# Kernel optimization log

Hardware: AMD Instinct MI355X
Metric: run time of the kernel (lower is better)

## Reference

```python
import jax, jax.numpy as jnp
import numpy as np
from jax import lax

H = 1024
D = 128
T = 64  # n_step + n_middle


def gru_cell(x, h, w_ih, w_hh, b_ih, b_hh):
    # torch.nn.GRUCell gate order: r, z, n
    gi = x @ w_ih.T + b_ih
    gh = h @ w_hh.T + b_hh
    ir, iz, i_n = jnp.split(gi, 3, axis=-1)
    hr, hz, h_n = jnp.split(gh, 3, axis=-1)
    r = jax.nn.sigmoid(ir + hr)
    z = jax.nn.sigmoid(iz + hz)
    n = jnp.tanh(i_n + r * h_n)
    return (1.0 - z) * n + z * h


def decoder(z_seq, z8, n1, w_init, b_init, wi1, wh1, bi1, bh1, wi2, wh2, bi2, bh2, w_out, b_out):
    B = z_seq.shape[0]
    out0 = jnp.zeros((B, D), z_seq.dtype).at[:, -1].set(1.0)
    h0 = z8 @ w_init.T + b_init              # [B, H]
    h1 = jnp.zeros_like(h0)                  # replaced at i == 0
    xs = (jnp.arange(T), jnp.swapaxes(z_seq, 0, 1))  # ([T], [T, B, D])

    def step(carry, x):
        h0, h1, out = carry
        i, z_i = x
        inp = jnp.where(i <= n1 - 1, z_i, out)
        h0n = gru_cell(inp, h0, wi1, wh1, bi1, bh1)
        h1 = jnp.where(i == 0, h0n, h1)
        h1n = gru_cell(h0n, h1, wi2, wh2, bi2, bh2)
        out = h1n @ w_out.T + b_out          # [B, 128]
        return (h0n, h1n, out), out

    _, outs = lax.scan(step, (h0, h1, out0), xs)  # [T, B, 128]
    return jnp.swapaxes(outs[n1 - 1:], 0, 1)      # [B, T-n1+1, 128]


def _p(key, shape):
    return jax.random.normal(key, shape, dtype=jnp.float32) * 0.02


def setup_inputs() -> dict:
    key = jax.random.key(0)
    ks = jax.random.split(key, 32)
    B = 2048
    inp = {
        'zp': jax.random.normal(ks[0], (B, T, D), jnp.float32),
        'zr': jax.random.normal(ks[1], (B, T, D), jnp.float32),
        'zp8': jax.random.normal(ks[2], (B, D), jnp.float32),
        'zr8': jax.random.normal(ks[3], (B, D), jnp.float32),
        'n1': 16,
        'n2': 48,
    }
    # GRU cells 1..4: (w_ih [3H, in], w_hh [3H, H], b_ih [3H], b_hh [3H])
    for j, name in enumerate(['1', '2', '3', '4']):
        in_dim = D if name in ('1', '3') else H
        inp['wi' + name] = _p(ks[4 + 4 * j], (3 * H, in_dim))
        inp['wh' + name] = _p(ks[5 + 4 * j], (3 * H, H))
        inp['bi' + name] = _p(ks[6 + 4 * j], (3 * H,))
        inp['bh' + name] = _p(ks[7 + 4 * j], (3 * H,))
    inp['w_init0'] = _p(ks[20], (H, D)); inp['b_init0'] = _p(ks[21], (H,))
    inp['w_init1'] = _p(ks[22], (H, D)); inp['b_init1'] = _p(ks[23], (H,))
    inp['w_out0'] = _p(ks[24], (D, H)); inp['b_out0'] = _p(ks[25], (D,))
    inp['w_out1'] = _p(ks[26], (D, H)); inp['b_out1'] = _p(ks[27], (D,))
    return inp


def reference(zp, zr, zp8, zr8, n1, n2,
              wi1, wh1, bi1, bh1, wi2, wh2, bi2, bh2,
              wi3, wh3, bi3, bh3, wi4, wh4, bi4, bh4,
              w_init0, b_init0, w_init1, b_init1,
              w_out0, b_out0, w_out1, b_out1):
    z_r = decoder(zr, zr8, n1, w_init0, b_init0, wi1, wh1, bi1, bh1,
                  wi2, wh2, bi2, bh2, w_out0, b_out0)
    z_p = decoder(zp, zp8, n1, w_init1, b_init1, wi3, wh3, bi3, bh3,
                  wi4, wh4, bi4, bh4, w_out1, b_out1)
    return (z_p, z_r)
```

## Files before the change

### kernel.cpp

```cpp
#include <hip/hip_runtime.h>

typedef unsigned short u16;
typedef unsigned int u32;
typedef __attribute__((ext_vector_type(8))) short short8;
typedef __attribute__((ext_vector_type(4))) float f32x4;

#define DEV __device__ __forceinline__

DEV u16 f2bf(float f){
  u32 u = __builtin_bit_cast(u32, f);
  u += 0x7fffu + ((u >> 16) & 1u);
  return (u16)(u >> 16);
}
DEV float sigm(float x){ return 1.f / (1.f + __expf(-x)); }
DEV float tanh_(float x){ return 2.f / (1.f + __expf(-2.f * x)) - 1.f; }

DEV void gl_lds16(const void* g, void* l){
  __builtin_amdgcn_global_load_lds(
      (const __attribute__((address_space(1))) u32*)g,
      (__attribute__((address_space(3))) u32*)l, 16, 0, 0);
}

#define MFMA16(A,B,C) __builtin_amdgcn_mfma_f32_16x16x32_bf16(A, B, C, 0, 0, 0)

__global__ void pack_w_kernel(const float* __restrict__ wi, const float* __restrict__ wh,
                              u16* __restrict__ dst, int Ki, int Kh, int nrows){
  const int KT = Ki + Kh;
  const long n = (long)nrows * KT;
  for (long idx = (long)blockIdx.x * blockDim.x + threadIdx.x; idx < n;
       idx += (long)gridDim.x * blockDim.x){
    int r = (int)(idx / KT), c = (int)(idx % KT);
    float v = (c < Ki) ? wi[(long)r * Ki + c] : wh[(long)r * Kh + (c - Ki)];
    dst[idx] = f2bf(v);
  }
}

struct InitA { const float* z8; const float* wini; const float* bini; float* h0f; u16* h0bf; };

__global__ __launch_bounds__(256)
void init_kernel(InitA A0, InitA A1){
  const InitA& a = (blockIdx.z == 0) ? A0 : A1;
  __shared__ float lz[64][128];
  const int tid = threadIdx.x;
  const int rb = blockIdx.x * 64, ub = blockIdx.y * 128;
  {
    const int row = tid >> 2, q = tid & 3;
    const float4* p = (const float4*)(a.z8 + (long)(rb + row) * 128 + q * 32);
    float4* dst = (float4*)&lz[row][q * 32];
    #pragma unroll
    for (int j = 0; j < 8; ++j) dst[j] = p[j];
  }
  __syncthreads();
  const int u = ub + (tid & 127);
  const int rg = tid >> 7;
  float acc[32];
  #pragma unroll
  for (int r = 0; r < 32; ++r) acc[r] = 0.f;
  for (int k = 0; k < 128; k += 4){
    float4 w4 = *(const float4*)&a.wini[(long)u * 128 + k];
    #pragma unroll
    for (int r = 0; r < 32; ++r){
      float4 z4 = *(const float4*)&lz[rg * 32 + r][k];
      acc[r] += w4.x * z4.x + w4.y * z4.y + w4.z * z4.z + w4.w * z4.w;
    }
  }
  const float b = a.bini[u];
  #pragma unroll
  for (int r = 0; r < 32; ++r){
    const long row = rb + rg * 32 + r;
    const float v = acc[r] + b;
    a.h0f[row * 1024 + u] = v;
    a.h0bf[row * 1024 + u] = f2bf(v);
  }
}

struct CellA {
  const u16* W;
  const float* bi; const float* bh;
  const float* afz; const float* afo;
  const u16* ab1; const u16* ab2;
  const float* holdr; float* holdw; u16* hbfw;
};

struct Frags { short8 af[2][4]; short8 bg[2][3][2]; };

template<int CELL>
__global__ __launch_bounds__(512, 1)
void cell_kernel(CellA A0, CellA A1, const int* dn1, int step){
  constexpr int KTOT = (CELL == 1) ? 1152 : 2048;
  constexpr int KT = KTOT / 64;
  constexpr int NI_STEPS = (CELL == 1) ? 2 : 16;

  __shared__ u16 lA[2][256 * 64];
  __shared__ u16 lB[2][192 * 64];

  const CellA& a = (blockIdx.y == 0) ? A0 : A1;
  const int tid = threadIdx.x;
  const int lane = tid & 63;
  const int wv = tid >> 6;
  const int wm = wv >> 1;
  const int wn = wv & 1;
  const int bid = blockIdx.x;
  const int m_idx = (bid >> 3) & 7;
  const int n_idx = ((bid & 7) << 1) | (bid >> 6);
  const int brow = m_idx * 256;
  const int u0 = n_idx * 64;

  f32x4 aR[4][2] = {}; f32x4 aZ[4][2] = {};
  f32x4 aNI[4][2] = {}; f32x4 aNH[4][2] = {};

  const int srow = tid >> 3;
  const int sxor8 = ((tid & 7) ^ (srow & 7)) * 8;

  auto stage = [&](int bf, int kt){
    const int k0 = kt * 64;
    const u16* ab; int kk;
    if constexpr (CELL == 1){ ab = a.ab1; kk = k0 - 128; }
    else { if (k0 < 1024){ ab = a.ab1; kk = k0; } else { ab = a.ab2; kk = k0 - 1024; } }
    #pragma unroll
    for (int j = 0; j < 4; ++j)
      gl_lds16(ab + (long)(brow + j * 64 + srow) * 1024 + kk + sxor8,
               &lA[bf][(j * 64 + wv * 8) * 64]);
    #pragma unroll
    for (int g = 0; g < 3; ++g)
      gl_lds16(a.W + (long)(g * 1024 + u0 + srow) * KTOT + k0 + sxor8,
               &lB[bf][(g * 64 + wv * 8) * 64]);
  };

  const int l15 = lane & 15;
  const int kq = lane >> 4;
  const int sx = lane & 7;

  auto loadf = [&](int bf, Frags& F){
    #pragma unroll
    for (int ks = 0; ks < 2; ++ks){
      const int soff = (((ks * 4 + kq) ^ sx)) * 8;
      #pragma unroll
      for (int fr = 0; fr < 4; ++fr)
        F.af[ks][fr] = *(const short8*)&lA[bf][(wm * 64 + fr * 16 + l15) * 64 + soff];
      #pragma unroll
      for (int g = 0; g < 3; ++g)
        #pragma unroll
        for (int fc = 0; fc < 2; ++fc)
          F.bg[ks][g][fc] = *(const short8*)&lB[bf][(g * 64 + wn * 32 + fc * 16 + l15) * 64 + soff];
    }
  };

  auto domfma = [&](Frags& F, bool toNI){
    #pragma unroll
    for (int ks = 0; ks < 2; ++ks){
      #pragma unroll
      for (int fr = 0; fr < 4; ++fr)
        #pragma unroll
        for (int fc = 0; fc < 2; ++fc){
          aR[fr][fc] = MFMA16(F.af[ks][fr], F.bg[ks][0][fc], aR[fr][fc]);
          aZ[fr][fc] = MFMA16(F.af[ks][fr], F.bg[ks][1][fc], aZ[fr][fc]);
        }
      if (toNI){
        #pragma unroll
        for (int fr = 0; fr < 4; ++fr)
          #pragma unroll
          for (int fc = 0; fc < 2; ++fc)
            aNI[fr][fc] = MFMA16(F.af[ks][fr], F.bg[ks][2][fc], aNI[fr][fc]);
      } else {
        #pragma unroll
        for (int fr = 0; fr < 4; ++fr)
          #pragma unroll
          for (int fc = 0; fc < 2; ++fc)
            aNH[fr][fc] = MFMA16(F.af[ks][fr], F.bg[ks][2][fc], aNH[fr][fc]);
      }
    }
  };

  int kstart;
  if constexpr (CELL == 1){
    const int n1v = *dn1;
    const float* fsrc; long fstr;
    if (step < n1v){ fsrc = a.afz; fstr = 64 * 128; }
    else           { fsrc = a.afo; fstr = 128; }
    {
      const int row = tid >> 1, half = tid & 1;
      #pragma unroll
      for (int st = 0; st < 2; ++st){
        const float* pp = fsrc + (long)(brow + row) * fstr + st * 64 + half * 32;
        #pragma unroll
        for (int q = 0; q < 4; ++q){
          float4 x = ((const float4*)pp)[2 * q];
          float4 y = ((const float4*)pp)[2 * q + 1];
          short8 o;
          o[0] = (short)f2bf(x.x); o[1] = (short)f2bf(x.y);
          o[2] = (short)f2bf(x.z); o[3] = (short)f2bf(x.w);
          o[4] = (short)f2bf(y.x); o[5] = (short)f2bf(y.y);
          o[6] = (short)f2bf(y.z); o[7] = (short)f2bf(y.w);
          const int s = half * 4 + q;
          *(short8*)&lA[st][row * 64 + ((s ^ (row & 7)) * 8)] = o;
        }
        #pragma unroll
        for (int g = 0; g < 3; ++g)
          gl_lds16(a.W + (long)(g * 1024 + u0 + srow) * KTOT + st * 64 + sxor8,
                   &lB[st][(g * 64 + wv * 8) * 64]);
      }
    }
    __syncthreads();
    { Frags F; loadf(0, F); domfma(F, true); }
    { Frags F; loadf(1, F); domfma(F, true); }
    __syncthreads();
    stage(0, 2); stage(1, 3);
    kstart = 2;
  } else {
    stage(0, 0); stage(1, 1);
    kstart = 0;
  }

  for (int kt = kstart; kt < KT; ++kt){
    const int b = kt & 1;
    if (kt < KT - 1) asm volatile("s_waitcnt vmcnt(7)" ::: "memory");
    else             asm volatile("s_waitcnt vmcnt(0)" ::: "memory");
    __builtin_amdgcn_s_barrier();
    Frags F;
    loadf(b, F);
    asm volatile("s_waitcnt lgkmcnt(0)" ::: "memory");
    __builtin_amdgcn_s_barrier();
    if (kt + 2 < KT) stage(b, kt + 2);
    __builtin_amdgcn_s_setprio(1);
    domfma(F, kt < NI_STEPS);
    __builtin_amdgcn_s_setprio(0);
  }

  const int rq = (lane >> 4) * 4;
  #pragma unroll
  for (int fc = 0; fc < 2; ++fc){
    const int u = u0 + wn * 32 + fc * 16 + l15;
    const float br = a.bi[u] + a.bh[u];
    const float bz = a.bi[1024 + u] + a.bh[1024 + u];
    const float bni = a.bi[2048 + u];
    const float bnh = a.bh[2048 + u];
    #pragma unroll
    for (int fr = 0; fr < 4; ++fr){
      #pragma unroll
      for (int rg = 0; rg < 4; ++rg){
        const long row = brow + wm * 64 + fr * 16 + rq + rg;
        const float r = sigm(aR[fr][fc][rg] + br);
        const float z = sigm(aZ[fr][fc][rg] + bz);
        const float n = tanh_(aNI[fr][fc][rg] + bni + r * (aNH[fr][fc][rg] + bnh));
        const float hp = a.holdr[row * 1024 + u];
        const float hn = (1.f - z) * n + z * hp;
        a.holdw[row * 1024 + u] = hn;
        a.hbfw[row * 1024 + u] = f2bf(hn);
      }
    }
  }
}

struct OutA { const u16* Ah; const u16* Wo; const float* bo; float* outf; };

__global__ __launch_bounds__(256, 2)
void out_kernel(OutA A0, OutA A1, const int* dn1, int step, float* __restrict__ dout, long outhalf){
  const int n1v = *dn1;
  if (step < n1v - 1) return;
  __shared__ u16 lA[2][32 * 64];
  __shared__ u16 lB[2][128 * 64];
  const OutA& a = (blockIdx.y == 0) ? A0 : A1;
  const int tid = threadIdx.x, lane = tid & 63, wv = tid >> 6;
  const int brow = blockIdx.x * 32;
  f32x4 acc[2][2] = {};
  const int srow = tid >> 3;
  const int sxor8 = ((tid & 7) ^ (srow & 7)) * 8;

  auto stage = [&](int bf, int kt){
    const int k0 = kt * 64;
    gl_lds16(a.Ah + (long)(brow + srow) * 1024 + k0 + sxor8, &lA[bf][wv * 8 * 64]);
    #pragma unroll
    for (int j = 0; j < 4; ++j)
      gl_lds16(a.Wo + (long)(j * 32 + srow) * 1024 + k0 + sxor8,
               &lB[bf][(j * 32 + wv * 8) * 64]);
  };

  stage(0, 0); stage(1, 1);
  const int l15 = lane & 15, kq = lane >> 4, sx = lane & 7;
  for (int kt = 0; kt < 16; ++kt){
    const int b = kt & 1;
    if (kt < 15) asm volatile("s_waitcnt vmcnt(5)" ::: "memory");
    else         asm volatile("s_waitcnt vmcnt(0)" ::: "memory");
    __builtin_amdgcn_s_barrier();
    short8 af[2][2], bf2[2][2];
    #pragma unroll
    for (int ks = 0; ks < 2; ++ks){
      const int soff = (((ks * 4 + kq) ^ sx)) * 8;
      af[ks][0] = *(const short8*)&lA[b][(l15) * 64 + soff];
      af[ks][1] = *(const short8*)&lA[b][(16 + l15) * 64 + soff];
      bf2[ks][0] = *(const short8*)&lB[b][(wv * 32 + l15) * 64 + soff];
      bf2[ks][1] = *(const short8*)&lB[b][(wv * 32 + 16 + l15) * 64 + soff];
    }
    asm volatile("s_waitcnt lgkmcnt(0)" ::: "memory");
    __builtin_amdgcn_s_barrier();
    if (kt + 2 < 16) stage(b, kt + 2);
    __builtin_amdgcn_s_setprio(1);
    #pragma unroll
    for (int ks = 0; ks < 2; ++ks)
      #pragma unroll
      for (int fr = 0; fr < 2; ++fr)
        #pragma unroll
        for (int fc = 0; fc < 2; ++fc)
          acc[fr][fc] = MFMA16(af[ks][fr], bf2[ks][fc], acc[fr][fc]);
    __builtin_amdgcn_s_setprio(0);
  }
  const int nst = 65 - n1v;
  const int t = step - (n1v - 1);
  const int rq = (lane >> 4) * 4;
  #pragma unroll
  for (int fc = 0; fc < 2; ++fc){
    const int u = wv * 32 + fc * 16 + l15;
    const float bo = a.bo[u];
    #pragma unroll
    for (int fr = 0; fr < 2; ++fr){
      #pragma unroll
      for (int rg = 0; rg < 4; ++rg){
        const long row = brow + fr * 16 + rq + rg;
        const float v = acc[fr][fc][rg] + bo;
        a.outf[row * 128 + u] = v;
        dout[(long)blockIdx.y * outhalf + (row * nst + t) * 128 + u] = v;
      }
    }
  }
}

extern "C" void kernel_launch(void* const* d_in, const int* in_sizes, int n_in,
                              void* d_out, int out_size, void* d_ws, size_t ws_size,
                              hipStream_t stream){
  const float* zz[2]   = { (const float*)d_in[0],  (const float*)d_in[1] };
  const float* z8[2]   = { (const float*)d_in[2],  (const float*)d_in[3] };
  const int* dn1       = (const int*)d_in[4];
  const float* wi_c1[2] = { (const float*)d_in[14], (const float*)d_in[6] };
  const float* wh_c1[2] = { (const float*)d_in[15], (const float*)d_in[7] };
  const float* bi_c1[2] = { (const float*)d_in[16], (const float*)d_in[8] };
  const float* bh_c1[2] = { (const float*)d_in[17], (const float*)d_in[9] };
  const float* wi_c2[2] = { (const float*)d_in[18], (const float*)d_in[10] };
  const float* wh_c2[2] = { (const float*)d_in[19], (const float*)d_in[11] };
  const float* bi_c2[2] = { (const float*)d_in[20], (const float*)d_in[12] };
  const float* bh_c2[2] = { (const float*)d_in[21], (const float*)d_in[13] };
  const float* wini[2]  = { (const float*)d_in[24], (const float*)d_in[22] };
  const float* bini[2]  = { (const float*)d_in[25], (const float*)d_in[23] };
  const float* wout[2]  = { (const float*)d_in[28], (const float*)d_in[26] };
  const float* bout[2]  = { (const float*)d_in[29], (const float*)d_in[27] };

  char* p = (char*)d_ws;
  auto alloc = [&](size_t bytes)->char*{
    char* q = p; p += (bytes + 255) & ~(size_t)255; return q;
  };
  u16* W1c[2]; u16* W2c[2]; u16* Woc[2];
  float* h0f[2]; float* h1f[2]; float* outf[2];
  u16* h0bf[2][2]; u16* h1bf[2][2];
  for (int d = 0; d < 2; ++d){
    W1c[d] = (u16*)alloc(3072ULL * 1152 * 2);
    W2c[d] = (u16*)alloc(3072ULL * 2048 * 2);
    Woc[d] = (u16*)alloc(128ULL * 1024 * 2);
    h0f[d] = (float*)alloc(2048ULL * 1024 * 4);
    h1f[d] = (float*)alloc(2048ULL * 1024 * 4);
    outf[d] = (float*)alloc(2048ULL * 128 * 4);
    for (int b = 0; b < 2; ++b){
      h0bf[d][b] = (u16*)alloc(2048ULL * 1024 * 2);
      h1bf[d][b] = (u16*)alloc(2048ULL * 1024 * 2);
    }
  }
  if ((size_t)(p - (char*)d_ws) > ws_size) return;

  for (int d = 0; d < 2; ++d){
    pack_w_kernel<<<dim3(1024), dim3(256), 0, stream>>>(wi_c1[d], wh_c1[d], W1c[d], 128, 1024, 3072);
    pack_w_kernel<<<dim3(1024), dim3(256), 0, stream>>>(wi_c2[d], wh_c2[d], W2c[d], 1024, 1024, 3072);
    pack_w_kernel<<<dim3(64),   dim3(256), 0, stream>>>(wout[d], wout[d], Woc[d], 1024, 0, 128);
  }
  {
    InitA I0{ z8[0], wini[0], bini[0], h0f[0], h0bf[0][0] };
    InitA I1{ z8[1], wini[1], bini[1], h0f[1], h0bf[1][0] };
    init_kernel<<<dim3(32, 8, 2), dim3(256), 0, stream>>>(I0, I1);
  }

  const long outhalf = (long)out_size / 2;

  for (int i = 0; i < 64; ++i){
    const int cur = i & 1, nxt = cur ^ 1;
    CellA c1[2], c2[2];
    for (int d = 0; d < 2; ++d){
      c1[d] = CellA{ W1c[d], bi_c1[d], bh_c1[d],
                     zz[d] + (long)i * 128, outf[d],
                     h0bf[d][cur], nullptr,
                     h0f[d], h0f[d], h0bf[d][nxt] };
      c2[d] = CellA{ W2c[d], bi_c2[d], bh_c2[d],
                     nullptr, nullptr,
                     h0bf[d][nxt], (i == 0) ? h0bf[d][nxt] : h1bf[d][cur],
                     (i == 0) ? h0f[d] : h1f[d], h1f[d], h1bf[d][nxt] };
    }
    cell_kernel<1><<<dim3(128, 2), dim3(512), 0, stream>>>(c1[0], c1[1], dn1, i);
    cell_kernel<2><<<dim3(128, 2), dim3(512), 0, stream>>>(c2[0], c2[1], dn1, i);
    OutA o0{ h1bf[0][nxt], Woc[0], bout[0], outf[0] };
    OutA o1{ h1bf[1][nxt], Woc[1], bout[1], outf[1] };
    out_kernel<<<dim3(64, 2), dim3(256), 0, stream>>>(o0, o1, dn1, i, (float*)d_out, outhalf);
  }
}
```

Baseline: 6.807 ms.

## Interleave per-gate LDS fragment reads with MFMAs and pin schedule with sched barriers

Splits the fragment load into separate A and per-gate B reads, then issues the R and Z gate MFMAs while later B fragments are still arriving, using partial lgkmcnt waits. sched_barrier fences keep the compiler from reordering across the hand-placed waits and barriers. Launch bounds become amdgpu_waves_per_eu(2,2), which changes the register budget. The intent is to hide LDS read latency behind MFMA work. The risk is that the tighter register budget or the rigid schedule causes spills or stalls.

Measured after the change: 6.813 ms. About the same (+0.1%).

```diff
diff --git a/kernel.cpp b/kernel.cpp
--- a/kernel.cpp
+++ b/kernel.cpp
@@ -6,6 +6,7 @@
 typedef __attribute__((ext_vector_type(4))) float f32x4;
 
 #define DEV __device__ __forceinline__
+#define SB0() __builtin_amdgcn_sched_barrier(0)
 
 DEV u16 f2bf(float f){
   u32 u = __builtin_bit_cast(u32, f);
@@ -82,10 +83,8 @@
   const float* holdr; float* holdw; u16* hbfw;
 };
 
-struct Frags { short8 af[2][4]; short8 bg[2][3][2]; };
-
 template<int CELL>
-__global__ __launch_bounds__(512, 1)
+__global__ __attribute__((amdgpu_waves_per_eu(2, 2))) __launch_bounds__(512)
 void cell_kernel(CellA A0, CellA A1, const int* dn1, int step){
   constexpr int KTOT = (CELL == 1) ? 1152 : 2048;
   constexpr int KT = KTOT / 64;
@@ -131,45 +130,32 @@
   const int kq = lane >> 4;
   const int sx = lane & 7;
 
-  auto loadf = [&](int bf, Frags& F){
+  auto read_a = [&](int bf, short8 (&af)[2][4]){
     #pragma unroll
     for (int ks = 0; ks < 2; ++ks){
       const int soff = (((ks * 4 + kq) ^ sx)) * 8;
       #pragma unroll
       for (int fr = 0; fr < 4; ++fr)
-        F.af[ks][fr] = *(const short8*)&lA[bf][(wm * 64 + fr * 16 + l15) * 64 + soff];
-      #pragma unroll
-      for (int g = 0; g < 3; ++g)
+        af[ks][fr] = *(const short8*)&lA[bf][(wm * 64 + fr * 16 + l15) * 64 + soff];
+    }
+  };
+  auto read_b = [&](int bf, int g, short8 (&bg)[2][2]){
+    #pragma unroll
+    for (int ks = 0; ks < 2; ++ks){
+      const int soff = (((ks * 4 + kq) ^ sx)) * 8;
+      #pragma unroll
+      for (int fc = 0; fc < 2; ++fc)
+        bg[ks][fc] = *(const short8*)&lB[bf][(g * 64 + wn * 32 + fc * 16 + l15) * 64 + soff];
+    }
+  };
+  auto mfma_gate = [&](const short8 (&af)[2][4], const short8 (&bg)[2][2], f32x4 (&A)[4][2]){
+    #pragma unroll
+    for (int ks = 0; ks < 2; ++ks)
+      #pragma unroll
+      for (int fr = 0; fr < 4; ++fr)
         #pragma unroll
         for (int fc = 0; fc < 2; ++fc)
-          F.bg[ks][g][fc] = *(const short8*)&lB[bf][(g * 64 + wn * 32 + fc * 16 + l15) * 64 + soff];
-    }
-  };
-
-  auto domfma = [&](Frags& F, bool toNI){
-    #pragma unroll
-    for (int ks = 0; ks < 2; ++ks){
-      #pragma unroll
-      for (int fr = 0; fr < 4; ++fr)
-        #pragma unroll
-        for (int fc = 0; fc < 2; ++fc){
-          aR[fr][fc] = MFMA16(F.af[ks][fr], F.bg[ks][0][fc], aR[fr][fc]);
-          aZ[fr][fc] = MFMA16(F.af[ks][fr], F.bg[ks][1][fc], aZ[fr][fc]);
-        }
-      if (toNI){
-        #pragma unroll
-        for (int fr = 0; fr < 4; ++fr)
-          #pragma unroll
-          for (int fc = 0; fc < 2; ++fc)
-            aNI[fr][fc] = MFMA16(F.af[ks][fr], F.bg[ks][2][fc], aNI[fr][fc]);
-      } else {
-        #pragma unroll
-        for (int fr = 0; fr < 4; ++fr)
-          #pragma unroll
-          for (int fc = 0; fc < 2; ++fc)
-            aNH[fr][fc] = MFMA16(F.af[ks][fr], F.bg[ks][2][fc], aNH[fr][fc]);
-      }
-    }
+          A[fr][fc] = MFMA16(af[ks][fr], bg[ks][fc], A[fr][fc]);
   };
 
   int kstart;
@@ -202,8 +188,20 @@
       }
     }
     __syncthreads();
-    { Frags F; loadf(0, F); domfma(F, true); }
-    { Frags F; loadf(1, F); domfma(F, true); }
+    #pragma unroll
+    for (int st = 0; st < 2; ++st){
+      short8 af[2][4], bg[2][2];
+      read_a(st, af);
+      read_b(st, 0, bg);
+      asm volatile("s_waitcnt lgkmcnt(0)" ::: "memory"); SB0();
+      mfma_gate(af, bg, aR);
+      read_b(st, 1, bg);
+      asm volatile("s_waitcnt lgkmcnt(0)" ::: "memory"); SB0();
+      mfma_gate(af, bg, aZ);
+      read_b(st, 2, bg);
+      asm volatile("s_waitcnt lgkmcnt(0)" ::: "memory"); SB0();
+      mfma_gate(af, bg, aNI);
+    }
     __syncthreads();
     stage(0, 2); stage(1, 3);
     kstart = 2;
@@ -216,14 +214,29 @@
     const int b = kt & 1;
     if (kt < KT - 1) asm volatile("s_waitcnt vmcnt(7)" ::: "memory");
     else             asm volatile("s_waitcnt vmcnt(0)" ::: "memory");
+    SB0();
     __builtin_amdgcn_s_barrier();
-    Frags F;
-    loadf(b, F);
-    asm volatile("s_waitcnt lgkmcnt(0)" ::: "memory");
+    SB0();
+    short8 af[2][4], b0[2][2], b1[2][2], b2[2][2];
+    read_a(b, af);    SB0();
+    read_b(b, 0, b0); SB0();
+    read_b(b, 1, b1); SB0();
+    asm volatile("s_waitcnt lgkmcnt(4)" ::: "memory"); SB0();
+    __builtin_amdgcn_s_setprio(1);
+    mfma_gate(af, b0, aR);
+    __builtin_amdgcn_s_setprio(0);
+    read_b(b, 2, b2); SB0();
+    asm volatile("s_waitcnt lgkmcnt(4)" ::: "memory"); SB0();
+    __builtin_amdgcn_s_setprio(1);
+    mfma_gate(af, b1, aZ);
+    __builtin_amdgcn_s_setprio(0);
+    asm volatile("s_waitcnt lgkmcnt(0)" ::: "memory"); SB0();
     __builtin_amdgcn_s_barrier();
+    SB0();
     if (kt + 2 < KT) stage(b, kt + 2);
     __builtin_amdgcn_s_setprio(1);
-    domfma(F, kt < NI_STEPS);
+    if (kt < NI_STEPS) mfma_gate(af, b2, aNI);
+    else               mfma_gate(af, b2, aNH);
     __builtin_amdgcn_s_setprio(0);
   }
 
@@ -282,7 +295,9 @@
     const int b = kt & 1;
     if (kt < 15) asm volatile("s_waitcnt vmcnt(5)" ::: "memory");
     else         asm volatile("s_waitcnt vmcnt(0)" ::: "memory");
+    SB0();
     __builtin_amdgcn_s_barrier();
+    SB0();
     short8 af[2][2], bf2[2][2];
     #pragma unroll
     for (int ks = 0; ks < 2; ++ks){
@@ -292,8 +307,9 @@
       bf2[ks][0] = *(const short8*)&lB[b][(wv * 32 + l15) * 64 + soff];
       bf2[ks][1] = *(const short8*)&lB[b][(wv * 32 + 16 + l15) * 64 + soff];
     }
-    asm volatile("s_waitcnt lgkmcnt(0)" ::: "memory");
+    asm volatile("s_waitcnt lgkmcnt(0)" ::: "memory"); SB0();
     __builtin_amdgcn_s_barrier();
+    SB0();
     if (kt + 2 < 16) stage(b, kt + 2);
     __builtin_amdgcn_s_setprio(1);
     #pragma unroll
```

## Pre-swizzle weights and hidden states into MFMA fragment order, load directly to registers

Applied to the files above, without the earlier changes.

Weights are packed and hidden-state bf16 copies are written in a layout that matches the MFMA fragment order. Both GEMMs then load operands straight from global memory into registers with a software-pipelined double buffer, replacing LDS staging and the barriers around it. The output GEMM is retiled so each block covers 64 rows with 8 column fragments per wave, which halves its grid. This removes LDS traffic and synchronisation, but every wave now loads its own copy of the weights without sharing through LDS, and the code depends on global-load latency being hidden by the two-stage register pipeline at 2 waves per EU.

After: 7.431 ms. 9.2% more time.

```diff
diff --git a/kernel.cpp b/kernel.cpp
--- a/kernel.cpp
+++ b/kernel.cpp
@@ -6,6 +6,7 @@
 typedef __attribute__((ext_vector_type(4))) float f32x4;
 
 #define DEV __device__ __forceinline__
+#define SB0() __builtin_amdgcn_sched_barrier(0)
 
 DEV u16 f2bf(float f){
   u32 u = __builtin_bit_cast(u32, f);
@@ -15,24 +16,30 @@
 DEV float sigm(float x){ return 1.f / (1.f + __expf(-x)); }
 DEV float tanh_(float x){ return 2.f / (1.f + __expf(-2.f * x)) - 1.f; }
 
-DEV void gl_lds16(const void* g, void* l){
-  __builtin_amdgcn_global_load_lds(
-      (const __attribute__((address_space(1))) u32*)g,
-      (__attribute__((address_space(3))) u32*)l, 16, 0, 0);
-}
-
 #define MFMA16(A,B,C) __builtin_amdgcn_mfma_f32_16x16x32_bf16(A, B, C, 0, 0, 0)
+
 
 __global__ void pack_w_kernel(const float* __restrict__ wi, const float* __restrict__ wh,
                               u16* __restrict__ dst, int Ki, int Kh, int nrows){
   const int KT = Ki + Kh;
+  const int KB = KT >> 5;
   const long n = (long)nrows * KT;
   for (long idx = (long)blockIdx.x * blockDim.x + threadIdx.x; idx < n;
        idx += (long)gridDim.x * blockDim.x){
-    int r = (int)(idx / KT), c = (int)(idx % KT);
-    float v = (c < Ki) ? wi[(long)r * Ki + c] : wh[(long)r * Kh + (c - Ki)];
+    const int e = (int)(idx & 7);
+    const int lane = (int)((idx >> 3) & 63);
+    const long t = idx >> 9;
+    const int kb = (int)(t % KB);
+    const int rb = (int)(t / KB);
+    const int r = rb * 16 + (lane & 15);
+    const int k = kb * 32 + (lane >> 4) * 8 + e;
+    float v = (k < Ki) ? wi[(long)r * Ki + k] : wh[(long)r * Kh + (k - Ki)];
     dst[idx] = f2bf(v);
   }
+}
+
+DEV long hfrag_idx(int row, int u){
+  return ((long)((row >> 4) * 32 + (u >> 5)) * 64 + (row & 15) + ((u >> 3) & 3) * 16) * 8 + (u & 7);
 }
 
 struct InitA { const float* z8; const float* wini; const float* bini; float* h0f; u16* h0bf; };
@@ -70,7 +77,7 @@
     const long row = rb + rg * 32 + r;
     const float v = acc[r] + b;
     a.h0f[row * 1024 + u] = v;
-    a.h0bf[row * 1024 + u] = f2bf(v);
+    a.h0bf[hfrag_idx((int)row, u)] = f2bf(v);
   }
 }
 
@@ -82,17 +89,15 @@
   const float* holdr; float* holdw; u16* hbfw;
 };
 
-struct Frags { short8 af[2][4]; short8 bg[2][3][2]; };
-
 template<int CELL>
-__global__ __launch_bounds__(512, 1)
+__global__ __attribute__((amdgpu_waves_per_eu(2, 2))) __launch_bounds__(512)
 void cell_kernel(CellA A0, CellA A1, const int* dn1, int step){
   constexpr int KTOT = (CELL == 1) ? 1152 : 2048;
   constexpr int KT = KTOT / 64;
+  constexpr int KBW = KTOT / 32;
   constexpr int NI_STEPS = (CELL == 1) ? 2 : 16;
 
-  __shared__ u16 lA[2][256 * 64];
-  __shared__ u16 lB[2][192 * 64];
+  __shared__ u16 lA[(CELL == 1) ? (2 * 256 * 64) : 64];
 
   const CellA& a = (blockIdx.y == 0) ? A0 : A1;
   const int tid = threadIdx.x;
@@ -101,76 +106,60 @@
   const int wm = wv >> 1;
   const int wn = wv & 1;
   const int bid = blockIdx.x;
-  const int m_idx = (bid >> 3) & 7;
-  const int n_idx = ((bid & 7) << 1) | (bid >> 6);
+  const int inner = bid >> 3;
+  const int m_idx = inner & 7;
+  const int n_idx = (bid & 7) * 2 + (inner >> 3);
   const int brow = m_idx * 256;
   const int u0 = n_idx * 64;
 
   f32x4 aR[4][2] = {}; f32x4 aZ[4][2] = {};
   f32x4 aNI[4][2] = {}; f32x4 aNH[4][2] = {};
 
-  const int srow = tid >> 3;
-  const int sxor8 = ((tid & 7) ^ (srow & 7)) * 8;
-
-  auto stage = [&](int bf, int kt){
-    const int k0 = kt * 64;
-    const u16* ab; int kk;
-    if constexpr (CELL == 1){ ab = a.ab1; kk = k0 - 128; }
-    else { if (k0 < 1024){ ab = a.ab1; kk = k0; } else { ab = a.ab2; kk = k0 - 1024; } }
-    #pragma unroll
-    for (int j = 0; j < 4; ++j)
-      gl_lds16(ab + (long)(brow + j * 64 + srow) * 1024 + kk + sxor8,
-               &lA[bf][(j * 64 + wv * 8) * 64]);
+  const int rbA0 = (brow >> 4) + wm * 4;
+  const int rbW0 = (u0 >> 4) + wn * 2;
+
+  auto ldA = [&](int kt, int ks, short8 (&af)[4]){
+    const u16* m; int kb;
+    if constexpr (CELL == 1){ m = a.ab1; kb = kt * 2 - 4 + ks; }
+    else { if (kt < 16){ m = a.ab1; kb = kt * 2 + ks; } else { m = a.ab2; kb = (kt - 16) * 2 + ks; } }
+    #pragma unroll
+    for (int fr = 0; fr < 4; ++fr)
+      af[fr] = *(const short8*)(m + (((long)(rbA0 + fr) * 32 + kb) * 64 + lane) * 8);
+  };
+  auto ldB = [&](int kt, int ks, short8 (&bg)[6]){
+    const int kb = kt * 2 + ks;
     #pragma unroll
     for (int g = 0; g < 3; ++g)
-      gl_lds16(a.W + (long)(g * 1024 + u0 + srow) * KTOT + k0 + sxor8,
-               &lB[bf][(g * 64 + wv * 8) * 64]);
+      #pragma unroll
+      for (int fc = 0; fc < 2; ++fc)
+        bg[g * 2 + fc] = *(const short8*)(a.W + (((long)(g * 64 + rbW0 + fc) * KBW + kb) * 64 + lane) * 8);
+  };
+  auto mfmaHalf = [&](const short8 (&af)[4], const short8 (&bg)[6], bool toNI){
+    #pragma unroll
+    for (int fr = 0; fr < 4; ++fr)
+      #pragma unroll
+      for (int fc = 0; fc < 2; ++fc){
+        aR[fr][fc] = MFMA16(af[fr], bg[0 + fc], aR[fr][fc]);
+        aZ[fr][fc] = MFMA16(af[fr], bg[2 + fc], aZ[fr][fc]);
+      }
+    if (toNI){
+      #pragma unroll
+      for (int fr = 0; fr < 4; ++fr)
+        #pragma unroll
+        for (int fc = 0; fc < 2; ++fc)
+          aNI[fr][fc] = MFMA16(af[fr], bg[4 + fc], aNI[fr][fc]);
+    } else {
+      #pragma unroll
+      for (int fr = 0; fr < 4; ++fr)
+        #pragma unroll
+        for (int fc = 0; fc < 2; ++fc)
+          aNH[fr][fc] = MFMA16(af[fr], bg[4 + fc], aNH[fr][fc]);
+    }
   };
 
   const int l15 = lane & 15;
   const int kq = lane >> 4;
   const int sx = lane & 7;
-
-  auto loadf = [&](int bf, Frags& F){
-    #pragma unroll
-    for (int ks = 0; ks < 2; ++ks){
-      const int soff = (((ks * 4 + kq) ^ sx)) * 8;
-      #pragma unroll
-      for (int fr = 0; fr < 4; ++fr)
-        F.af[ks][fr] = *(const short8*)&lA[bf][(wm * 64 + fr * 16 + l15) * 64 + soff];
-      #pragma unroll
-      for (int g = 0; g < 3; ++g)
-        #pragma unroll
-        for (int fc = 0; fc < 2; ++fc)
-          F.bg[ks][g][fc] = *(const short8*)&lB[bf][(g * 64 + wn * 32 + fc * 16 + l15) * 64 + soff];
-    }
-  };
-
-  auto domfma = [&](Frags& F, bool toNI){
-    #pragma unroll
-    for (int ks = 0; ks < 2; ++ks){
-      #pragma unroll
-      for (int fr = 0; fr < 4; ++fr)
-        #pragma unroll
-        for (int fc = 0; fc < 2; ++fc){
-          aR[fr][fc] = MFMA16(F.af[ks][fr], F.bg[ks][0][fc], aR[fr][fc]);
-          aZ[fr][fc] = MFMA16(F.af[ks][fr], F.bg[ks][1][fc], aZ[fr][fc]);
-        }
-      if (toNI){
-        #pragma unroll
-        for (int fr = 0; fr < 4; ++fr)
-          #pragma unroll
-          for (int fc = 0; fc < 2; ++fc)
-            aNI[fr][fc] = MFMA16(F.af[ks][fr], F.bg[ks][2][fc], aNI[fr][fc]);
-      } else {
-        #pragma unroll
-        for (int fr = 0; fr < 4; ++fr)
-          #pragma unroll
-          for (int fc = 0; fc < 2; ++fc)
-            aNH[fr][fc] = MFMA16(F.af[ks][fr], F.bg[ks][2][fc], aNH[fr][fc]);
-      }
-    }
-  };
 
   int kstart;
   if constexpr (CELL == 1){
@@ -193,38 +182,49 @@
           o[4] = (short)f2bf(y.x); o[5] = (short)f2bf(y.y);
           o[6] = (short)f2bf(y.z); o[7] = (short)f2bf(y.w);
           const int s = half * 4 + q;
-          *(short8*)&lA[st][row * 64 + ((s ^ (row & 7)) * 8)] = o;
+          *(short8*)&lA[st * 256 * 64 + row * 64 + ((s ^ (row & 7)) * 8)] = o;
         }
+      }
+    }
+    __syncthreads();
+    #pragma unroll
+    for (int st = 0; st < 2; ++st){
+      short8 af0[4], af1[4], fb0[6], fb1[6];
+      #pragma unroll
+      for (int ks = 0; ks < 2; ++ks){
+        const int soff = (((ks * 4 + kq) ^ sx)) * 8;
         #pragma unroll
-        for (int g = 0; g < 3; ++g)
-          gl_lds16(a.W + (long)(g * 1024 + u0 + srow) * KTOT + st * 64 + sxor8,
-                   &lB[st][(g * 64 + wv * 8) * 64]);
+        for (int fr = 0; fr < 4; ++fr)
+          (ks ? af1 : af0)[fr] = *(const short8*)&lA[st * 256 * 64 + (wm * 64 + fr * 16 + l15) * 64 + soff];
       }
-    }
-    __syncthreads();
-    { Frags F; loadf(0, F); domfma(F, true); }
-    { Frags F; loadf(1, F); domfma(F, true); }
-    __syncthreads();
-    stage(0, 2); stage(1, 3);
+      ldB(st, 0, fb0); ldB(st, 1, fb1);
+      asm volatile("s_waitcnt lgkmcnt(0) vmcnt(0)" ::: "memory"); SB0();
+      mfmaHalf(af0, fb0, true);
+      mfmaHalf(af1, fb1, true);
+    }
     kstart = 2;
   } else {
-    stage(0, 0); stage(1, 1);
     kstart = 0;
   }
 
+  short8 fa0[4], fb0[6], fa1[4], fb1[6];
+  ldA(kstart, 0, fa0); ldB(kstart, 0, fb0); SB0();
   for (int kt = kstart; kt < KT; ++kt){
-    const int b = kt & 1;
-    if (kt < KT - 1) asm volatile("s_waitcnt vmcnt(7)" ::: "memory");
-    else             asm volatile("s_waitcnt vmcnt(0)" ::: "memory");
-    __builtin_amdgcn_s_barrier();
-    Frags F;
-    loadf(b, F);
-    asm volatile("s_waitcnt lgkmcnt(0)" ::: "memory");
-    __builtin_amdgcn_s_barrier();
-    if (kt + 2 < KT) stage(b, kt + 2);
+    const bool toNI = (kt < NI_STEPS);
+    ldA(kt, 1, fa1); ldB(kt, 1, fb1); SB0();
+    asm volatile("s_waitcnt vmcnt(10)" ::: "memory"); SB0();
     __builtin_amdgcn_s_setprio(1);
-    domfma(F, kt < NI_STEPS);
-    __builtin_amdgcn_s_setprio(0);
+    mfmaHalf(fa0, fb0, toNI);
+    __builtin_amdgcn_s_setprio(0); SB0();
+    if (kt + 1 < KT){
+      ldA(kt + 1, 0, fa0); ldB(kt + 1, 0, fb0); SB0();
+      asm volatile("s_waitcnt vmcnt(10)" ::: "memory"); SB0();
+    } else {
+      asm volatile("s_waitcnt vmcnt(0)" ::: "memory"); SB0();
+    }
+    __builtin_amdgcn_s_setprio(1);
+    mfmaHalf(fa1, fb1, toNI);
+    __builtin_amdgcn_s_setprio(0); SB0();
   }
 
   const int rq = (lane >> 4) * 4;
@@ -239,14 +239,14 @@
     for (int fr = 0; fr < 4; ++fr){
       #pragma unroll
       for (int rg = 0; rg < 4; ++rg){
-        const long row = brow + wm * 64 + fr * 16 + rq + rg;
+        const int row = brow + wm * 64 + fr * 16 + rq + rg;
         const float r = sigm(aR[fr][fc][rg] + br);
         const float z = sigm(aZ[fr][fc][rg] + bz);
         const float n = tanh_(aNI[fr][fc][rg] + bni + r * (aNH[fr][fc][rg] + bnh));
-        const float hp = a.holdr[row * 1024 + u];
+        const float hp = a.holdr[(long)row * 1024 + u];
         const float hn = (1.f - z) * n + z * hp;
-        a.holdw[row * 1024 + u] = hn;
-        a.hbfw[row * 1024 + u] = f2bf(hn);
+        a.holdw[(long)row * 1024 + u] = hn;
+        a.hbfw[hfrag_idx(row, u)] = f2bf(hn);
       }
     }
   }
@@ -258,69 +258,55 @@
 void out_kernel(OutA A0, OutA A1, const int* dn1, int step, float* __restrict__ dout, long outhalf){
   const int n1v = *dn1;
   if (step < n1v - 1) return;
-  __shared__ u16 lA[2][32 * 64];
-  __shared__ u16 lB[2][128 * 64];
   const OutA& a = (blockIdx.y == 0) ? A0 : A1;
   const int tid = threadIdx.x, lane = tid & 63, wv = tid >> 6;
-  const int brow = blockIdx.x * 32;
-  f32x4 acc[2][2] = {};
-  const int srow = tid >> 3;
-  const int sxor8 = ((tid & 7) ^ (srow & 7)) * 8;
-
-  auto stage = [&](int bf, int kt){
-    const int k0 = kt * 64;
-    gl_lds16(a.Ah + (long)(brow + srow) * 1024 + k0 + sxor8, &lA[bf][wv * 8 * 64]);
-    #pragma unroll
-    for (int j = 0; j < 4; ++j)
-      gl_lds16(a.Wo + (long)(j * 32 + srow) * 1024 + k0 + sxor8,
-               &lB[bf][(j * 32 + wv * 8) * 64]);
-  };
-
-  stage(0, 0); stage(1, 1);
-  const int l15 = lane & 15, kq = lane >> 4, sx = lane & 7;
-  for (int kt = 0; kt < 16; ++kt){
-    const int b = kt & 1;
-    if (kt < 15) asm volatile("s_waitcnt vmcnt(5)" ::: "memory");
-    else         asm volatile("s_waitcnt vmcnt(0)" ::: "memory");
-    __builtin_amdgcn_s_barrier();
-    short8 af[2][2], bf2[2][2];
-    #pragma unroll
-    for (int ks = 0; ks < 2; ++ks){
-      const int soff = (((ks * 4 + kq) ^ sx)) * 8;
-      af[ks][0] = *(const short8*)&lA[b][(l15) * 64 + soff];
-      af[ks][1] = *(const short8*)&lA[b][(16 + l15) * 64 + soff];
-      bf2[ks][0] = *(const short8*)&lB[b][(wv * 32 + l15) * 64 + soff];
-      bf2[ks][1] = *(const short8*)&lB[b][(wv * 32 + 16 + l15) * 64 + soff];
-    }
-    asm volatile("s_waitcnt lgkmcnt(0)" ::: "memory");
-    __builtin_amdgcn_s_barrier();
-    if (kt + 2 < 16) stage(b, kt + 2);
-    __builtin_amdgcn_s_setprio(1);
-    #pragma unroll
-    for (int ks = 0; ks < 2; ++ks)
-      #pragma unroll
-      for (int fr = 0; fr < 2; ++fr)
-        #pragma unroll
-        for (int fc = 0; fc < 2; ++fc)
-          acc[fr][fc] = MFMA16(af[ks][fr], bf2[ks][fc], acc[fr][fc]);
-    __builtin_amdgcn_s_setprio(0);
-  }
+  const int brow = blockIdx.x * 64;
+  const int rbA = (brow >> 4) + wv;
+  f32x4 acc[8] = {};
+
+  auto ldA1 = [&](int kb)->short8 {
+    return *(const short8*)(a.Ah + (((long)rbA * 32 + kb) * 64 + lane) * 8);
+  };
+  auto ldBo = [&](int kb, short8 (&fb)[8]){
+    #pragma unroll
+    for (int j = 0; j < 8; ++j)
+      fb[j] = *(const short8*)(a.Wo + (((long)j * 32 + kb) * 64 + lane) * 8);
+  };
+  auto mm = [&](const short8& fa, const short8 (&fb)[8]){
+    #pragma unroll
+    for (int fc = 0; fc < 8; ++fc)
+      acc[fc] = MFMA16(fa, fb[fc], acc[fc]);
+  };
+
+  short8 fa0, fa1, fb0[8], fb1[8];
+  fa0 = ldA1(0); ldBo(0, fb0); SB0();
+  for (int kb = 0; kb < 32; kb += 2){
+    fa1 = ldA1(kb + 1); ldBo(kb + 1, fb1); SB0();
+    asm volatile("s_waitcnt vmcnt(9)" ::: "memory"); SB0();
+    __builtin_amdgcn_s_setprio(1); mm(fa0, fb0); __builtin_amdgcn_s_setprio(0); SB0();
+    if (kb + 2 < 32){
+      fa0 = ldA1(kb + 2); ldBo(kb + 2, fb0); SB0();
+      asm volatile("s_waitcnt vmcnt(9)" ::: "memory"); SB0();
+    } else {
+      asm volatile("s_waitcnt vmcnt(0)" ::: "memory"); SB0();
+    }
+    __builtin_amdgcn_s_setprio(1); mm(fa1, fb1); __builtin_amdgcn_s_setprio(0); SB0();
+  }
+
   const int nst = 65 - n1v;
   const int t = step - (n1v - 1);
+  const int l15 = lane & 15;
   const int rq = (lane >> 4) * 4;
   #pragma unroll
-  for (int fc = 0; fc < 2; ++fc){
-    const int u = wv * 32 + fc * 16 + l15;
+  for (int fc = 0; fc < 8; ++fc){
+    const int u = fc * 16 + l15;
     const float bo = a.bo[u];
     #pragma unroll
-    for (int fr = 0; fr < 2; ++fr){
-      #pragma unroll
-      for (int rg = 0; rg < 4; ++rg){
-        const long row = brow + fr * 16 + rq + rg;
-        const float v = acc[fr][fc][rg] + bo;
-        a.outf[row * 128 + u] = v;
-        dout[(long)blockIdx.y * outhalf + (row * nst + t) * 128 + u] = v;
-      }
+    for (int rg = 0; rg < 4; ++rg){
+      const long row = brow + wv * 16 + rq + rg;
+      const float v = acc[fc][rg] + bo;
+      a.outf[row * 128 + u] = v;
+      dout[(long)blockIdx.y * outhalf + (row * nst + t) * 128 + u] = v;
     }
   }
 }
@@ -395,6 +381,6 @@
     cell_kernel<2><<<dim3(128, 2), dim3(512), 0, stream>>>(c2[0], c2[1], dn1, i);
     OutA o0{ h1bf[0][nxt], Woc[0], bout[0], outf[0] };
     OutA o1{ h1bf[1][nxt], Woc[1], bout[1], outf[1] };
-    out_kernel<<<dim3(64, 2), dim3(256), 0, stream>>>(o0, o1, dn1, i, (float*)d_out, outhalf);
-  }
-}
+    out_kernel<<<dim3(32, 2), dim3(256), 0, stream>>>(o0, o1, dn1, i, (float*)d_out, outhalf);
+  }
+}
```
